# Performance work log

Hardware: AMD Instinct MI355X
Metric: run time of the kernel (lower is better)

The kernel has to match this reference:

```python
import jax, jax.numpy as jnp
import numpy as np

NUM_PAIRS, PAIR_DIM, MACRO_DIM, NUM_SLOTS, BATCH = 28, 128, 256, 64, 4096
D_ALL = NUM_PAIRS * PAIR_DIM  # 3584
EPS = 1e-5


def _layernorm(x, g, b):
    mu = jnp.mean(x, axis=-1, keepdims=True)
    var = jnp.mean(jnp.square(x - mu), axis=-1, keepdims=True)
    return (x - mu) * jax.lax.rsqrt(var + EPS) * g + b


def _memory_read(q, keys, values):
    # attention-style associative read: softmax(q K^T / sqrt(dk)) V
    dk = keys.shape[-1]
    scores = jnp.einsum('bd,sd->bs', q, keys) / jnp.sqrt(jnp.asarray(dk, q.dtype))
    attn = jax.nn.softmax(scores, axis=-1)
    return jnp.einsum('bs,sv->bv', attn, values)


def setup_inputs() -> dict:
    key = jax.random.key(0)
    ks = jax.random.split(key, 12)
    s = lambda k, shape, scale=0.02: jax.random.normal(k, shape, dtype=jnp.float32) * scale
    return {
        'pair_states': jax.random.normal(ks[0], (BATCH, NUM_PAIRS, PAIR_DIM), dtype=jnp.float32),
        'macro_state': jax.random.normal(ks[1], (BATCH, MACRO_DIM), dtype=jnp.float32),
        'mem_pair_keys': s(ks[2], (NUM_SLOTS, PAIR_DIM)),
        'mem_pair_vals': s(ks[3], (NUM_SLOTS, D_ALL)),
        'mem_macro_keys': s(ks[4], (NUM_SLOTS, MACRO_DIM)),
        'mem_macro_vals': s(ks[5], (NUM_SLOTS, D_ALL)),
        'fusion_w1': s(ks[6], (2 * D_ALL, D_ALL)),
        'fusion_b1': jnp.zeros((D_ALL,), jnp.float32),
        'fusion_ln_g': jnp.ones((D_ALL,), jnp.float32),
        'fusion_ln_b': jnp.zeros((D_ALL,), jnp.float32),
        'fusion_w2': s(ks[7], (D_ALL, D_ALL)),
        'fusion_b2': jnp.zeros((D_ALL,), jnp.float32),
        'pair_w': s(ks[8], (NUM_PAIRS, 2 * PAIR_DIM, PAIR_DIM)),
        'pair_b': jnp.zeros((NUM_PAIRS, PAIR_DIM), jnp.float32),
        'pair_ln_g': jnp.ones((NUM_PAIRS, PAIR_DIM), jnp.float32),
        'pair_ln_b': jnp.zeros((NUM_PAIRS, PAIR_DIM), jnp.float32),
    }


def reference(pair_states, macro_state, mem_pair_keys, mem_pair_vals,
              mem_macro_keys, mem_macro_vals, fusion_w1, fusion_b1,
              fusion_ln_g, fusion_ln_b, fusion_w2, fusion_b2,
              pair_w, pair_b, pair_ln_g, pair_ln_b):
    B = pair_states.shape[0]
    # associative memory reads
    pair_query = jnp.mean(pair_states, axis=1)                       # (B, pair_dim)
    pair_corr = _memory_read(pair_query, mem_pair_keys, mem_pair_vals)   # (B, D_ALL)
    macro_corr = _memory_read(macro_state, mem_macro_keys, mem_macro_vals)  # (B, D_ALL)
    # fusion MLP: Linear -> LayerNorm -> GELU -> Linear
    h = jnp.concatenate([pair_corr, macro_corr], axis=-1) @ fusion_w1 + fusion_b1
    h = jax.nn.gelu(_layernorm(h, fusion_ln_g, fusion_ln_b), approximate=False)
    fused = (h @ fusion_w2 + fusion_b2).reshape(B, NUM_PAIRS, PAIR_DIM)
    # per-pair Linear + LayerNorm, batched over the pair axis
    x = jnp.concatenate([pair_states, fused], axis=-1)               # (B, P, 2*pair_dim)
    out = jnp.einsum('bpd,pde->bpe', x, pair_w) + pair_b
    return _layernorm(out, pair_ln_g, pair_ln_b)
```

## Files before the change

### kernel.cpp

```cpp
#include <hip/hip_runtime.h>
#include <hip/hip_bf16.h>
#include <math.h>


#define B_SZ  4096
#define NPAIR 28
#define PDIM  128
#define MDIM  256
#define NSLOT 64
#define DALL  3584
#define DCAT  7168
#define KS2   32
#define KCH2  224

typedef __hip_bfloat16 bf16;
typedef __attribute__((ext_vector_type(8))) short bf16x8;
typedef __attribute__((ext_vector_type(4))) short short4v;
typedef __attribute__((ext_vector_type(4))) float f32x4;

#define BARRIER() asm volatile("s_barrier" ::: "memory")
#define LGKM0()   asm volatile("s_waitcnt lgkmcnt(0)" ::: "memory")
#define VMCNT4()  asm volatile("s_waitcnt vmcnt(4)" ::: "memory")
#define VMCNT0()  asm volatile("s_waitcnt vmcnt(0)" ::: "memory")

__device__ __forceinline__ void async_copy16(void* lds, const void* g) {
  __builtin_amdgcn_global_load_lds((__attribute__((address_space(1))) void*)g,
                                   (__attribute__((address_space(3))) void*)lds,
                                   16, 0, 0);
}

__global__ __launch_bounds__(512, 2)
void gemm224(const bf16* __restrict__ A, const bf16* __restrict__ Bt,
             bf16* __restrict__ Cout, const float* __restrict__ bias) {
  __shared__ __align__(16) char smem[131072];
  const int tid = threadIdx.x;
  const int wid = tid >> 6, lane = tid & 63;
  const int lr = lane & 15, lk = lane >> 4;
  const int wm = wid >> 1, wn = wid & 1;
  const int swz = ((int)blockIdx.x & 7) * 32 + ((int)blockIdx.x >> 3);
  const int bx = swz & 15, by = swz >> 4;
  const int col0 = bx * 224, row0 = by * 256;

  char* sA = smem;
  char* sB = smem + 65536;

  const int srow = tid >> 3;
  const int sg = (tid & 7) ^ (srow & 7);
  const bf16* aStage = A + (long)(row0 + srow) * DALL + sg * 8;
  const bf16* bStage = Bt + (long)(col0 + srow) * DALL + sg * 8;
  const int wOff = wid << 10;

  const int NT = DALL >> 6;

  const int sx = lr & 7;
  const int arowb = wm * 64 + lr;
  const int browb = wn * 112 + lr;

  f32x4 acc[4][7];
  const f32x4 zero = {0.f, 0.f, 0.f, 0.f};
#pragma unroll
  for (int m = 0; m < 4; ++m)
#pragma unroll
    for (int n = 0; n < 7; ++n) acc[m][n] = zero;

#pragma unroll
  for (int i = 0; i < 4; ++i)
    async_copy16(sB + i * 8192 + wOff, bStage + (long)i * 64 * DALL);
#pragma unroll
  for (int i = 0; i < 4; ++i)
    async_copy16(sA + i * 8192 + wOff, aStage + (long)i * 64 * DALL);
#pragma unroll
  for (int i = 0; i < 4; ++i)
    async_copy16(sB + 32768 + i * 8192 + wOff, bStage + (long)i * 64 * DALL + 64);
  VMCNT4();
  BARRIER();

  bf16x8 af[4][2], bf[7][2];

  for (int t = 0; t < NT; ++t) {
    const int cur = t & 1;
    char* cA = sA + cur * 32768;
    char* cB = sB + cur * 32768;
    char* nA = sA + (cur ^ 1) * 32768;

    if (t + 1 < NT) {
      const bf16* g = aStage + (long)(t + 1) * 64;
#pragma unroll
      for (int i = 0; i < 4; ++i)
        async_copy16(nA + i * 8192 + wOff, g + (long)i * 64 * DALL);
    }
#pragma unroll
    for (int m = 0; m < 4; ++m)
#pragma unroll
      for (int kk = 0; kk < 2; ++kk)
        af[m][kk] = *(const bf16x8*)(cA + (arowb + m * 16) * 128 +
                                     ((((kk << 2) | lk) ^ sx) << 4));
#pragma unroll
    for (int n = 0; n < 7; ++n)
#pragma unroll
      for (int kk = 0; kk < 2; ++kk)
        bf[n][kk] = *(const bf16x8*)(cB + (browb + n * 16) * 128 +
                                     ((((kk << 2) | lk) ^ sx) << 4));
    __builtin_amdgcn_s_setprio(1);
#pragma unroll
    for (int m = 0; m < 4; ++m)
#pragma unroll
      for (int n = 0; n < 4; ++n)
#pragma unroll
        for (int kk = 0; kk < 2; ++kk)
          acc[m][n] = __builtin_amdgcn_mfma_f32_16x16x32_bf16(
              af[m][kk], bf[n][kk], acc[m][n], 0, 0, 0);
    __builtin_amdgcn_s_setprio(0);
    LGKM0();
    BARRIER();

    const int more = (t + 2 < NT);
    if (more) {
      const bf16* g = bStage + (long)(t + 2) * 64;
#pragma unroll
      for (int i = 0; i < 4; ++i)
        async_copy16(cB + i * 8192 + wOff, g + (long)i * 64 * DALL);
    }
    __builtin_amdgcn_s_setprio(1);
#pragma unroll
    for (int m = 0; m < 4; ++m)
#pragma unroll
      for (int n = 4; n < 7; ++n)
#pragma unroll
        for (int kk = 0; kk < 2; ++kk)
          acc[m][n] = __builtin_amdgcn_mfma_f32_16x16x32_bf16(
              af[m][kk], bf[n][kk], acc[m][n], 0, 0, 0);
    __builtin_amdgcn_s_setprio(0);
    if (more) { VMCNT4(); } else { VMCNT0(); }
    BARRIER();
  }

#pragma unroll
  for (int m = 0; m < 4; ++m) {
#pragma unroll
    for (int n = 0; n < 7; ++n) {
      const int gc = col0 + wn * 112 + n * 16 + lr;
      const float bia = bias[gc];
#pragma unroll
      for (int j = 0; j < 4; ++j) {
        const int gr = row0 + wm * 64 + m * 16 + lk * 4 + j;
        Cout[(long)gr * DALL + gc] = __float2bfloat16(acc[m][n][j] + bia);
      }
    }
  }
}

__global__ __launch_bounds__(256)
void keyt_kernel(const float* __restrict__ pkeys, const float* __restrict__ mkeys,
                 float* __restrict__ pkT, float* __restrict__ mkT) {
  const int tid = threadIdx.x;
  if (blockIdx.x == 0) {
    for (int i = tid; i < PDIM * NSLOT; i += 256) {
      const int d = i >> 6, s = i & 63;
      pkT[i] = pkeys[s * PDIM + d];
    }
  } else {
    const int b = (int)blockIdx.x - 1;
    for (int i = b * 8192 + tid; i < (b + 1) * 8192; i += 256) {
      const int d = i >> 6, s = i & 63;
      mkT[i] = mkeys[s * MDIM + d];
    }
  }
}

__global__ __launch_bounds__(256)
void all_conv(const float* __restrict__ pv, const float* __restrict__ mv,
              bf16* __restrict__ pvb, bf16* __restrict__ mvb,
              const float* __restrict__ pw, bf16* __restrict__ pwTb,
              const float* __restrict__ w2, bf16* __restrict__ w2t,
              const float* __restrict__ ps, const float* __restrict__ mac,
              const float* __restrict__ pkT, const float* __restrict__ mkT,
              bf16* __restrict__ psb, bf16* __restrict__ att) {
  __shared__ __align__(16) char lsmem[9728];
  const int idx = blockIdx.x, tid = threadIdx.x;
  if (idx >= 4256) {
    float* q = (float*)lsmem;
    float* mrow = q + PDIM;
    float (*red)[PDIM] = (float(*)[PDIM])(mrow + MDIM);
    const int b = idx - 4256;
    const float* prow = ps + (long)b * DALL;
    if (tid < MDIM) mrow[tid] = mac[(long)b * MDIM + tid];
    float a8[8];
#pragma unroll
    for (int j = 0; j < 8; ++j) a8[j] = 0.f;
    for (int i = tid * 8; i < DALL; i += 2048) {
      float4 a = *(const float4*)(prow + i);
      float4 c = *(const float4*)(prow + i + 4);
      union { bf16 h[8]; bf16x8 v; } u;
      u.h[0] = __float2bfloat16(a.x); u.h[1] = __float2bfloat16(a.y);
      u.h[2] = __float2bfloat16(a.z); u.h[3] = __float2bfloat16(a.w);
      u.h[4] = __float2bfloat16(c.x); u.h[5] = __float2bfloat16(c.y);
      u.h[6] = __float2bfloat16(c.z); u.h[7] = __float2bfloat16(c.w);
      *(bf16x8*)(psb + (long)b * DALL + i) = u.v;
      a8[0] += a.x; a8[1] += a.y; a8[2] += a.z; a8[3] += a.w;
      a8[4] += c.x; a8[5] += c.y; a8[6] += c.z; a8[7] += c.w;
    }
    {
      float* rp = &red[tid >> 4][(tid & 15) * 8];
      *(f32x4*)rp = *(f32x4*)&a8[0];
      *(f32x4*)(rp + 4) = *(f32x4*)&a8[4];
    }
    __syncthreads();
    if (tid < PDIM) {
      float s = 0.f;
#pragma unroll
      for (int k = 0; k < 16; ++k) s += red[k][tid];
      q[tid] = s * (1.f / NPAIR);
    }
    __syncthreads();
    const int wid = tid >> 6, lane = tid & 63;
    if (wid == 0) {
      float s0 = 0.f, s1 = 0.f, s2 = 0.f, s3 = 0.f;
#pragma unroll
      for (int d = 0; d < PDIM; d += 4) {
        s0 += q[d] * pkT[d * 64 + lane];
        s1 += q[d + 1] * pkT[(d + 1) * 64 + lane];
        s2 += q[d + 2] * pkT[(d + 2) * 64 + lane];
        s3 += q[d + 3] * pkT[(d + 3) * 64 + lane];
      }
      float sc = ((s0 + s1) + (s2 + s3)) * 0.08838834764831845f;
      float mx = sc;
#pragma unroll
      for (int m = 32; m; m >>= 1) mx = fmaxf(mx, __shfl_xor(mx, m));
      float e = expf(sc - mx);
      float ssum = e;
#pragma unroll
      for (int m = 32; m; m >>= 1) ssum += __shfl_xor(ssum, m);
      att[(long)b * 128 + lane] = __float2bfloat16(e / ssum);
    } else if (wid == 1) {
      float s0 = 0.f, s1 = 0.f, s2 = 0.f, s3 = 0.f;
#pragma unroll
      for (int d = 0; d < MDIM; d += 4) {
        s0 += mrow[d] * mkT[d * 64 + lane];
        s1 += mrow[d + 1] * mkT[(d + 1) * 64 + lane];
        s2 += mrow[d + 2] * mkT[(d + 2) * 64 + lane];
        s3 += mrow[d + 3] * mkT[(d + 3) * 64 + lane];
      }
      float sc = ((s0 + s1) + (s2 + s3)) * 0.0625f;
      float mx = sc;
#pragma unroll
      for (int m = 32; m; m >>= 1) mx = fmaxf(mx, __shfl_xor(mx, m));
      float e = expf(sc - mx);
      float ssum = e;
#pragma unroll
      for (int m = 32; m; m >>= 1) ssum += __shfl_xor(ssum, m);
      att[(long)b * 128 + 64 + lane] = __float2bfloat16(e / ssum);
    }
    return;
  }
  if (idx < 224) {
    const int sel = idx >= 112;
    const float* in = sel ? mv : pv;
    bf16* out = sel ? mvb : pvb;
    const int bx = sel ? idx - 112 : idx;
    const int i = (bx * 256 + tid) * 8;
    float4 a = *(const float4*)(in + i);
    float4 b = *(const float4*)(in + i + 4);
    union { bf16 h[8]; bf16x8 v; } u;
    u.h[0] = __float2bfloat16(a.x); u.h[1] = __float2bfloat16(a.y);
    u.h[2] = __float2bfloat16(a.z); u.h[3] = __float2bfloat16(a.w);
    u.h[4] = __float2bfloat16(b.x); u.h[5] = __float2bfloat16(b.y);
    u.h[6] = __float2bfloat16(b.z); u.h[7] = __float2bfloat16(b.w);
    *(bf16x8*)(out + i) = u.v;
    return;
  }
  if (idx < 1120) {
    float (*tile)[33] = (float(*)[33])lsmem;
    const int t = idx - 224;
    const int c0 = (t & 3) * 32;
    const int r0 = ((t >> 2) & 7) * 32;
    const long base = (long)(t >> 5) * (MDIM * PDIM);
    const int tx = tid & 31, ty = tid >> 5;
#pragma unroll
    for (int i = 0; i < 4; ++i)
      tile[ty + i * 8][tx] = pw[base + (long)(r0 + ty + i * 8) * PDIM + c0 + tx];
    __syncthreads();
    const int cl = tid >> 3, rq = (tid & 7) * 4;
    union { bf16 h[4]; short4v v; } u;
#pragma unroll
    for (int j = 0; j < 4; ++j) u.h[j] = __float2bfloat16(tile[rq + j][cl]);
    *(short4v*)(pwTb + base + (long)(c0 + cl) * MDIM + r0 + rq) = u.v;
    return;
  }
  {
    bf16 (*s64)[72] = (bf16(*)[72])lsmem;
    const int t = idx - 1120;
    const int c0 = (t % 56) * 64, r0 = (t / 56) * 64;
    const int rr = tid >> 4, cc = (tid & 15) * 4;
#pragma unroll
    for (int i = 0; i < 4; ++i) {
      float4 v = *(const float4*)(w2 + (long)(r0 + rr + i * 16) * DALL + c0 + cc);
      union { bf16 h[4]; short4v s; } u;
      u.h[0] = __float2bfloat16(v.x); u.h[1] = __float2bfloat16(v.y);
      u.h[2] = __float2bfloat16(v.z); u.h[3] = __float2bfloat16(v.w);
      *(short4v*)&s64[rr + i * 16][cc] = u.s;
    }
    __syncthreads();
    const int oq = tid >> 6, oc = tid & 63;
    union { bf16 h[16]; bf16x8 v[2]; } u;
#pragma unroll
    for (int j = 0; j < 16; ++j) u.h[j] = s64[oq * 16 + j][oc];
    bf16* dst = w2t + (long)(c0 + oc) * DALL + r0 + oq * 16;
    *(bf16x8*)dst = u.v[0];
    *(bf16x8*)(dst + 8) = u.v[1];
  }
}

__global__ __launch_bounds__(256)
void precompute_direct(const float* __restrict__ w1, const bf16* __restrict__ pvb,
                       const bf16* __restrict__ mvb, float* __restrict__ part) {
  __shared__ __align__(16) bf16 sAt[256 * 40];
  __shared__ __align__(16) bf16 sBt[64 * 32];
  const int tid = threadIdx.x, wid = tid >> 6, lane = tid & 63;
  const int lr = lane & 15, lk = lane >> 4;
  const int n0 = blockIdx.x * 256;
  const int ksb = blockIdx.y;
  const int kbase = ksb * KCH2;
  const bf16* vb = (ksb < 16) ? pvb : mvb;
  const int kcol0 = (ksb < 16) ? kbase : kbase - DALL;

  const int bs = tid >> 2;
  const int bgs = (tid & 3) ^ (bs & 3);

  f32x4 acc[4][4];
  const f32x4 zero = {0.f, 0.f, 0.f, 0.f};
#pragma unroll
  for (int m = 0; m < 4; ++m)
#pragma unroll
    for (int n = 0; n < 4; ++n) acc[m][n] = zero;

  for (int kt = 0; kt < KCH2; kt += 32) {
    __syncthreads();
    {
      const float* src = w1 + (long)(kbase + kt) * DALL + n0 + tid;
      bf16* dst = sAt + tid * 40;
#pragma unroll
      for (int r8 = 0; r8 < 32; r8 += 4) {
        union { bf16 h[4]; short4v v; } u;
#pragma unroll
        for (int j = 0; j < 4; ++j)
          u.h[j] = __float2bfloat16(src[(long)(r8 + j) * DALL]);
        *(short4v*)(dst + r8) = u.v;
      }
    }
    async_copy16((char*)sBt + tid * 16,
                 vb + (long)bs * DALL + kcol0 + kt + bgs * 8);
    __syncthreads();
    bf16x8 af[4], bfr[4];
#pragma unroll
    for (int m = 0; m < 4; ++m)
      af[m] = *(const bf16x8*)((const char*)sAt +
                               ((wid * 64 + m * 16 + lr) * 40 + lk * 8) * 2);
#pragma unroll
    for (int n = 0; n < 4; ++n) {
      const int s = n * 16 + lr;
      bfr[n] = *(const bf16x8*)((const char*)sBt + s * 64 + ((lk ^ (s & 3)) << 4));
    }
#pragma unroll
    for (int m = 0; m < 4; ++m)
#pragma unroll
      for (int n = 0; n < 4; ++n)
        acc[m][n] =
            __builtin_amdgcn_mfma_f32_16x16x32_bf16(af[m], bfr[n], acc[m][n], 0, 0, 0);
  }
#pragma unroll
  for (int m = 0; m < 4; ++m)
#pragma unroll
    for (int n = 0; n < 4; ++n)
#pragma unroll
      for (int j = 0; j < 4; ++j) {
        const int gn = n0 + wid * 64 + m * 16 + lk * 4 + j;
        const int s = n * 16 + lr;
        part[((long)ksb * DALL + gn) * 64 + s] = acc[m][n][j];
      }
}

__global__ __launch_bounds__(256)
void reduce_cvt(const float* __restrict__ part, bf16* __restrict__ cvt) {
  const long i4 = ((long)blockIdx.x * 256 + threadIdx.x) * 4;
  const int n = (int)(i4 >> 7), sc = (int)(i4 & 127);
  const int half = sc >> 6, s0 = sc & 63;
  f32x4 s = {0.f, 0.f, 0.f, 0.f};
#pragma unroll
  for (int j = 0; j < 16; ++j)
    s += *(const f32x4*)(part + ((long)(half * 16 + j) * DALL + n) * 64 + s0);
#pragma unroll
  for (int k = 0; k < 4; ++k) cvt[i4 + k] = __float2bfloat16(s[k]);
}

__global__ __launch_bounds__(256)
void gemm_thin(const bf16* __restrict__ att, const bf16* __restrict__ cvt,
               bf16* __restrict__ hpre, const float* __restrict__ bias) {
  __shared__ __align__(16) bf16 sA[128 * 64];
  __shared__ __align__(16) bf16 sB[128 * 64];
  const int tid = threadIdx.x, wid = tid >> 6, lane = tid & 63;
  const int lr = lane & 15, lk = lane >> 4;
  const int col0 = blockIdx.x * 128, row0 = blockIdx.y * 128;
  const int srl = lane >> 3;
  const int sgl = (lane & 7) ^ srl;
  const int sx = lr & 7;

  f32x4 acc[2][8];
  const f32x4 zero = {0.f, 0.f, 0.f, 0.f};
#pragma unroll
  for (int m = 0; m < 2; ++m)
#pragma unroll
    for (int n = 0; n < 8; ++n) acc[m][n] = zero;

  for (int kt = 0; kt < 2; ++kt) {
    __syncthreads();
#pragma unroll
    for (int i = 0; i < 4; ++i) {
      const int r = i * 32 + wid * 8 + srl;
      async_copy16((char*)sA + i * 4096 + wid * 1024,
                   att + (long)(row0 + r) * 128 + kt * 64 + sgl * 8);
      async_copy16((char*)sB + i * 4096 + wid * 1024,
                   cvt + (long)(col0 + r) * 128 + kt * 64 + sgl * 8);
    }
    __syncthreads();
#pragma unroll
    for (int kk = 0; kk < 2; ++kk) {
      bf16x8 a0[2], b0[8];
      const int gb = (((kk << 2) | lk) ^ sx) << 4;
#pragma unroll
      for (int m = 0; m < 2; ++m)
        a0[m] = *(const bf16x8*)((const char*)sA + (wid * 32 + m * 16 + lr) * 128 + gb);
#pragma unroll
      for (int n = 0; n < 8; ++n)
        b0[n] = *(const bf16x8*)((const char*)sB + (n * 16 + lr) * 128 + gb);
#pragma unroll
      for (int m = 0; m < 2; ++m)
#pragma unroll
        for (int n = 0; n < 8; ++n)
          acc[m][n] = __builtin_amdgcn_mfma_f32_16x16x32_bf16(
              a0[m], b0[n], acc[m][n], 0, 0, 0);
    }
  }
#pragma unroll
  for (int m = 0; m < 2; ++m) {
#pragma unroll
    for (int n = 0; n < 8; ++n) {
      const int gc = col0 + n * 16 + lr;
      const float bia = bias[gc];
#pragma unroll
      for (int j = 0; j < 4; ++j) {
        const int gr = row0 + wid * 32 + m * 16 + lk * 4 + j;
        hpre[(long)gr * DALL + gc] = __float2bfloat16(acc[m][n][j] + bia);
      }
    }
  }
}

__global__ __launch_bounds__(256)
void ln_gelu_kernel(const bf16* __restrict__ h, const float* __restrict__ g,
                    const float* __restrict__ bb, bf16* __restrict__ h2) {
  const int row = blockIdx.x, tid = threadIdx.x;
  const bf16* x = h + (long)row * DALL;
  float v[14];
  float s1 = 0.f, s2 = 0.f;
#pragma unroll
  for (int i = 0; i < 14; ++i) {
    v[i] = __bfloat162float(x[i * 256 + tid]);
    s1 += v[i];
    s2 += v[i] * v[i];
  }
#pragma unroll
  for (int m = 32; m; m >>= 1) {
    s1 += __shfl_xor(s1, m);
    s2 += __shfl_xor(s2, m);
  }
  __shared__ float r1[4], r2[4];
  const int wid = tid >> 6, lane = tid & 63;
  if (lane == 0) {
    r1[wid] = s1;
    r2[wid] = s2;
  }
  __syncthreads();
  s1 = r1[0] + r1[1] + r1[2] + r1[3];
  s2 = r2[0] + r2[1] + r2[2] + r2[3];
  const float mean = s1 * (1.f / DALL);
  const float var = s2 * (1.f / DALL) - mean * mean;
  const float rstd = rsqrtf(var + 1e-5f);
#pragma unroll
  for (int i = 0; i < 14; ++i) {
    const int c = i * 256 + tid;
    const float y = (v[i] - mean) * rstd * g[c] + bb[c];
    const float ge = 0.5f * y * (1.f + erff(y * 0.7071067811865475f));
    h2[(long)row * DALL + c] = __float2bfloat16(ge);
  }
}

__global__ __launch_bounds__(256)
void pair_final(const bf16* __restrict__ psb, const bf16* __restrict__ fusedb,
                const bf16* __restrict__ pwT, const float* __restrict__ pb,
                const float* __restrict__ lng, const float* __restrict__ lnb,
                float* __restrict__ out) {
  __shared__ __align__(16) bf16 sA[128 * 64];
  __shared__ __align__(16) bf16 sB[128 * 64];
  const int tid = threadIdx.x, wid = tid >> 6, lane = tid & 63;
  const int lr = lane & 15, lk = lane >> 4;
  const int p = blockIdx.y, row0 = blockIdx.x * 128;
  const int srl = lane >> 3;
  const int sgl = (lane & 7) ^ srl;
  const int sx = lr & 7;
  const bf16* pwp = pwT + (long)p * (PDIM * MDIM);

  f32x4 acc[2][8];
  const f32x4 zero = {0.f, 0.f, 0.f, 0.f};
#pragma unroll
  for (int m = 0; m < 2; ++m)
#pragma unroll
    for (int n = 0; n < 8; ++n) acc[m][n] = zero;

  for (int kt = 0; kt < 4; ++kt) {
    __syncthreads();
    const bf16* Asrc = (kt < 2) ? psb : fusedb;
    const int acol = p * PDIM + (kt & 1) * 64;
#pragma unroll
    for (int i = 0; i < 4; ++i) {
      const int r = i * 32 + wid * 8 + srl;
      async_copy16((char*)sA + i * 4096 + wid * 1024,
                   Asrc + (long)(row0 + r) * DALL + acol + sgl * 8);
      async_copy16((char*)sB + i * 4096 + wid * 1024,
                   pwp + (long)r * MDIM + kt * 64 + sgl * 8);
    }
    __syncthreads();
#pragma unroll
    for (int kk = 0; kk < 2; ++kk) {
      bf16x8 a0[2], b0[8];
      const int gb = (((kk << 2) | lk) ^ sx) << 4;
#pragma unroll
      for (int m = 0; m < 2; ++m)
        a0[m] = *(const bf16x8*)((const char*)sA + (wid * 32 + m * 16 + lr) * 128 + gb);
#pragma unroll
      for (int n = 0; n < 8; ++n)
        b0[n] = *(const bf16x8*)((const char*)sB + (n * 16 + lr) * 128 + gb);
#pragma unroll
      for (int m = 0; m < 2; ++m)
#pragma unroll
        for (int n = 0; n < 8; ++n)
          acc[m][n] = __builtin_amdgcn_mfma_f32_16x16x32_bf16(
              a0[m], b0[n], acc[m][n], 0, 0, 0);
    }
  }
  float g_[8], b_[8], pb_[8];
#pragma unroll
  for (int n = 0; n < 8; ++n) {
    const int c = n * 16 + lr;
    g_[n] = lng[p * PDIM + c];
    b_[n] = lnb[p * PDIM + c];
    pb_[n] = pb[p * PDIM + c];
  }
#pragma unroll
  for (int m = 0; m < 2; ++m) {
#pragma unroll
    for (int j = 0; j < 4; ++j) {
      float vv[8];
      float s1 = 0.f, s2 = 0.f;
#pragma unroll
      for (int n = 0; n < 8; ++n) {
        vv[n] = acc[m][n][j] + pb_[n];
        s1 += vv[n];
        s2 += vv[n] * vv[n];
      }
#pragma unroll
      for (int msk = 1; msk <= 8; msk <<= 1) {
        s1 += __shfl_xor(s1, msk);
        s2 += __shfl_xor(s2, msk);
      }
      const float mean = s1 * (1.f / 128.f);
      const float var = s2 * (1.f / 128.f) - mean * mean;
      const float rstd = rsqrtf(var + 1e-5f);
      const int gr = row0 + wid * 32 + m * 16 + lk * 4 + j;
      float* orow = out + ((long)gr * NPAIR + p) * PDIM;
#pragma unroll
      for (int n = 0; n < 8; ++n)
        orow[n * 16 + lr] = (vv[n] - mean) * rstd * g_[n] + b_[n];
    }
  }
}

extern "C" void kernel_launch(void* const* d_in, const int* in_sizes, int n_in,
                              void* d_out, int out_size, void* d_ws, size_t ws_size,
                              hipStream_t stream) {
  (void)in_sizes; (void)n_in; (void)out_size; (void)ws_size;
  const float* ps   = (const float*)d_in[0];
  const float* mac  = (const float*)d_in[1];
  const float* pkey = (const float*)d_in[2];
  const float* pval = (const float*)d_in[3];
  const float* mkey = (const float*)d_in[4];
  const float* mval = (const float*)d_in[5];
  const float* w1   = (const float*)d_in[6];
  const float* b1   = (const float*)d_in[7];
  const float* lng1 = (const float*)d_in[8];
  const float* lnb1 = (const float*)d_in[9];
  const float* w2   = (const float*)d_in[10];
  const float* b2   = (const float*)d_in[11];
  const float* pw   = (const float*)d_in[12];
  const float* pb   = (const float*)d_in[13];
  const float* plng = (const float*)d_in[14];
  const float* plnb = (const float*)d_in[15];
  float* out = (float*)d_out;

  char* w = (char*)d_ws;
  size_t off = 0;
  auto carve = [&](size_t bytes) {
    char* pp = w + off;
    off += (bytes + 255) & ~(size_t)255;
    return pp;
  };
  bf16* psb   = (bf16*)carve((size_t)B_SZ * DALL * 2);
  bf16* w2t   = (bf16*)carve((size_t)(DALL + 32) * DALL * 2);
  bf16* pvb   = (bf16*)carve((size_t)NSLOT * DALL * 2);
  bf16* mvb   = (bf16*)carve((size_t)NSLOT * DALL * 2);
  bf16* pwTb  = (bf16*)carve((size_t)NPAIR * PDIM * MDIM * 2);
  bf16* att   = (bf16*)carve((size_t)B_SZ * 128 * 2);
  bf16* cvt   = (bf16*)carve((size_t)DALL * 128 * 2);
  float* part = (float*)carve((size_t)KS2 * DALL * 64 * 4);
  bf16* hpreb = (bf16*)carve((size_t)B_SZ * DALL * 2);
  bf16* h2    = (bf16*)carve((size_t)B_SZ * DALL * 2);
  float* pkT  = (float*)carve((size_t)PDIM * NSLOT * 4);
  float* mkT  = (float*)carve((size_t)MDIM * NSLOT * 4);
  bf16* fusedb = hpreb;

  keyt_kernel<<<dim3(3), 256, 0, stream>>>(pkey, mkey, pkT, mkT);
  all_conv<<<dim3(8352), 256, 0, stream>>>(pval, mval, pvb, mvb, pw, pwTb,
                                           w2, w2t, ps, mac, pkT, mkT, psb, att);
  precompute_direct<<<dim3(DALL / 256, KS2), 256, 0, stream>>>(w1, pvb, mvb, part);
  reduce_cvt<<<dim3(DALL * 128 / 1024), 256, 0, stream>>>(part, cvt);
  gemm_thin<<<dim3(DALL / 128, B_SZ / 128), 256, 0, stream>>>(att, cvt, hpreb, b1);
  ln_gelu_kernel<<<dim3(B_SZ), 256, 0, stream>>>(hpreb, lng1, lnb1, h2);
  gemm224<<<dim3(256), 512, 0, stream>>>(h2, w2t, fusedb, b2);
  pair_final<<<dim3(B_SZ / 128, NPAIR), 256, 0, stream>>>(
      psb, fusedb, pwTb, pb, plng, plnb, out);
}
```

Before: 246.0 us.

## Triple-buffer B tile and collapse GEMM main loop to one barrier per k-step

Changes the B-operand LDS buffering from a double buffer that was reused in place mid-iteration to a three-stage ring sized exactly for 224 rows. The first four waves load the leftover 32 rows, so the B prefetch no longer over-fetches 256 rows. A and B prefetches are now issued together after the fragment loads, and all 28 MFMAs per wave run back to back, which removes the mid-iteration barrier. LDS use rises to about 148KB per block, which may not fit two blocks per CU as launch_bounds requests and could lower occupancy. Waves now wait on different vmcnt values.

New measurement: 244.1 us (median of 2 runs). About the same (-0.8%).

```diff
diff --git a/kernel.cpp b/kernel.cpp
--- a/kernel.cpp
+++ b/kernel.cpp
@@ -21,6 +21,7 @@
 #define BARRIER() asm volatile("s_barrier" ::: "memory")
 #define LGKM0()   asm volatile("s_waitcnt lgkmcnt(0)" ::: "memory")
 #define VMCNT4()  asm volatile("s_waitcnt vmcnt(4)" ::: "memory")
+#define VMCNT3()  asm volatile("s_waitcnt vmcnt(3)" ::: "memory")
 #define VMCNT0()  asm volatile("s_waitcnt vmcnt(0)" ::: "memory")
 
 __device__ __forceinline__ void async_copy16(void* lds, const void* g) {
@@ -32,7 +33,7 @@
 __global__ __launch_bounds__(512, 2)
 void gemm224(const bf16* __restrict__ A, const bf16* __restrict__ Bt,
              bf16* __restrict__ Cout, const float* __restrict__ bias) {
-  __shared__ __align__(16) char smem[131072];
+  __shared__ __align__(16) char smem[151552];
   const int tid = threadIdx.x;
   const int wid = tid >> 6, lane = tid & 63;
   const int lr = lane & 15, lk = lane >> 4;
@@ -49,6 +50,7 @@
   const bf16* aStage = A + (long)(row0 + srow) * DALL + sg * 8;
   const bf16* bStage = Bt + (long)(col0 + srow) * DALL + sg * 8;
   const int wOff = wid << 10;
+  const int loWave = (wid < 4);
 
   const int NT = DALL >> 6;
 
@@ -65,30 +67,26 @@
 
 #pragma unroll
   for (int i = 0; i < 4; ++i)
+    async_copy16(sA + i * 8192 + wOff, aStage + (long)i * 64 * DALL);
+#pragma unroll
+  for (int i = 0; i < 3; ++i)
     async_copy16(sB + i * 8192 + wOff, bStage + (long)i * 64 * DALL);
-#pragma unroll
-  for (int i = 0; i < 4; ++i)
-    async_copy16(sA + i * 8192 + wOff, aStage + (long)i * 64 * DALL);
-#pragma unroll
-  for (int i = 0; i < 4; ++i)
-    async_copy16(sB + 32768 + i * 8192 + wOff, bStage + (long)i * 64 * DALL + 64);
-  VMCNT4();
+  if (loWave)
+    async_copy16(sB + 24576 + wOff, bStage + (long)192 * DALL);
+#pragma unroll
+  for (int i = 0; i < 3; ++i)
+    async_copy16(sB + 28672 + i * 8192 + wOff, bStage + (long)i * 64 * DALL + 64);
+  if (loWave)
+    async_copy16(sB + 28672 + 24576 + wOff, bStage + (long)192 * DALL + 64);
+  if (loWave) { VMCNT4(); } else { VMCNT3(); }
   BARRIER();
 
   bf16x8 af[4][2], bf[7][2];
 
   for (int t = 0; t < NT; ++t) {
-    const int cur = t & 1;
-    char* cA = sA + cur * 32768;
-    char* cB = sB + cur * 32768;
-    char* nA = sA + (cur ^ 1) * 32768;
-
-    if (t + 1 < NT) {
-      const bf16* g = aStage + (long)(t + 1) * 64;
-#pragma unroll
-      for (int i = 0; i < 4; ++i)
-        async_copy16(nA + i * 8192 + wOff, g + (long)i * 64 * DALL);
-    }
+    char* cA = sA + (t & 1) * 32768;
+    char* cB = sB + (t % 3) * 28672;
+
 #pragma unroll
     for (int m = 0; m < 4; ++m)
 #pragma unroll
@@ -101,37 +99,42 @@
       for (int kk = 0; kk < 2; ++kk)
         bf[n][kk] = *(const bf16x8*)(cB + (browb + n * 16) * 128 +
                                      ((((kk << 2) | lk) ^ sx) << 4));
+
+    if (t + 1 < NT) {
+      char* nA = sA + ((t + 1) & 1) * 32768;
+      const bf16* g = aStage + (long)(t + 1) * 64;
+#pragma unroll
+      for (int i = 0; i < 4; ++i)
+        async_copy16(nA + i * 8192 + wOff, g + (long)i * 64 * DALL);
+    }
+    const int more = (t + 2 < NT);
+    if (more) {
+      char* nB = sB + ((t + 2) % 3) * 28672;
+      const bf16* g = bStage + (long)(t + 2) * 64;
+#pragma unroll
+      for (int i = 0; i < 3; ++i)
+        async_copy16(nB + i * 8192 + wOff, g + (long)i * 64 * DALL);
+      if (loWave)
+        async_copy16(nB + 24576 + wOff, g + (long)192 * DALL);
+    }
+
     __builtin_amdgcn_s_setprio(1);
 #pragma unroll
     for (int m = 0; m < 4; ++m)
 #pragma unroll
-      for (int n = 0; n < 4; ++n)
+      for (int n = 0; n < 7; ++n)
 #pragma unroll
         for (int kk = 0; kk < 2; ++kk)
           acc[m][n] = __builtin_amdgcn_mfma_f32_16x16x32_bf16(
               af[m][kk], bf[n][kk], acc[m][n], 0, 0, 0);
     __builtin_amdgcn_s_setprio(0);
+
     LGKM0();
-    BARRIER();
-
-    const int more = (t + 2 < NT);
     if (more) {
-      const bf16* g = bStage + (long)(t + 2) * 64;
-#pragma unroll
-      for (int i = 0; i < 4; ++i)
-        async_copy16(cB + i * 8192 + wOff, g + (long)i * 64 * DALL);
-    }
-    __builtin_amdgcn_s_setprio(1);
-#pragma unroll
-    for (int m = 0; m < 4; ++m)
-#pragma unroll
-      for (int n = 4; n < 7; ++n)
-#pragma unroll
-        for (int kk = 0; kk < 2; ++kk)
-          acc[m][n] = __builtin_amdgcn_mfma_f32_16x16x32_bf16(
-              af[m][kk], bf[n][kk], acc[m][n], 0, 0, 0);
-    __builtin_amdgcn_s_setprio(0);
-    if (more) { VMCNT4(); } else { VMCNT0(); }
+      if (loWave) { VMCNT4(); } else { VMCNT3(); }
+    } else {
+      VMCNT0();
+    }
     BARRIER();
   }
 
```
